# Kernel optimization log

Hardware: AMD Instinct MI355X
Metric: run time of the kernel (lower is better)

The kernel has to match this reference:

```python
import jax, jax.numpy as jnp
import numpy as np

V, E, H, D = 32000, 512, 512, 3          # vocab, embed_dim, hidden_dim, max_depth
PD = max(H // 4, 16)                      # policy depth-embed dim = 128
DEPTH_EMBED_SCALE = 0.01
SIB_SCALE = 1.0 / np.sqrt(H)              # sibling_scale default 1/sqrt(hidden_dim)
GREEDY_THRESHOLD = 0.5
PROB_MIN, PROB_MAX = 1e-7, 1.0 - 1e-7


def _ln(x, g, b, eps=1e-5):
    m = x.mean(-1, keepdims=True)
    v = jnp.var(x, axis=-1, keepdims=True)
    return (x - m) * jax.lax.rsqrt(v + eps) * g + b


def setup_inputs() -> dict:
    key = jax.random.key(0)
    ks = jax.random.split(key, 12)
    def n(k, shape, s=0.02):
        return jax.random.normal(k, shape, jnp.float32) * s
    return {
        "token_ids": jax.random.randint(ks[0], (4096,), 0, V),
        "emb": n(ks[1], (V, E)),                      # embedding table
        "proj_w": n(ks[2], (H, E), 0.04), "proj_b": jnp.zeros(H, jnp.float32),
        "cf_w": n(ks[3], (2 * H, H), 0.04), "cf_b": jnp.zeros(2 * H, jnp.float32),
        "in_g": jnp.ones(H, jnp.float32), "in_b": jnp.zeros(H, jnp.float32),   # policy input LayerNorm
        "pde": n(ks[4], (D + 1, PD), 0.01),           # policy depth embedding
        "f1w": n(ks[5], (H // 2, H + PD), 0.04), "f1b": jnp.zeros(H // 2, jnp.float32),
        "n1g": jnp.ones(H // 2, jnp.float32), "n1b": jnp.zeros(H // 2, jnp.float32),
        "f2w": n(ks[6], (H // 4, H // 2), 0.06), "f2b": jnp.zeros(H // 4, jnp.float32),
        "n2g": jnp.ones(H // 4, jnp.float32), "n2b": jnp.zeros(H // 4, jnp.float32),
        "pow_w": n(ks[7], (1, H // 4), 0.01), "pow_b": jnp.zeros(1, jnp.float32),
        "sib": n(ks[8], (2, H)),                      # sibling embeddings (left/right)
        "dep": n(ks[9], (D + 1, H), 0.01),            # tree depth embeddings
        "out_w": n(ks[10], (V, H), 0.04), "out_b": jnp.zeros(V, jnp.float32),
    }


def _forward(token_ids, emb, proj_w, proj_b, cf_w, cf_b, in_g, in_b, pde,
             f1w, f1b, n1g, n1b, f2w, f2b, n2g, n2b, pow_w, pow_b,
             sib, dep, out_w, out_b):
    # h0: project token embeddings to hidden space. [N, H]
    h0 = emb[token_ids] @ proj_w.T + proj_b
    nodes = h0[None]                      # level-0 nodes: [1, N, H]
    agg_sum = h0                          # running sum over all tree nodes
    agg_cnt = jnp.float32(1.0)
    alive = jnp.float32(1.0)              # cumulative greedy-expand mask
    for level in range(D):
        # growth policy on the level-mean hidden (+ scaled depth embedding)
        lh = nodes.mean(0) + DEPTH_EMBED_SCALE * dep[level]          # [N, H]
        hn = _ln(lh, in_g, in_b)
        de = jnp.broadcast_to(pde[min(level, D)], (hn.shape[0], PD))
        x = jnp.concatenate([hn, de], axis=-1)
        x = jax.nn.relu(_ln(x @ f1w.T + f1b, n1g, n1b))
        x = jax.nn.relu(_ln(x @ f2w.T + f2b, n2g, n2b))
        p = jax.nn.sigmoid((x @ pow_w.T + pow_b)[..., 0])             # [N]
        p_mean = jnp.clip(p, PROB_MIN, PROB_MAX).mean()
        alive = alive * (p_mean >= GREEDY_THRESHOLD).astype(jnp.float32)
        # binary child expansion: child_fc then chunk into left/right + sibling embeds
        cf = jnp.einsum('mnh,kh->mnk', nodes, cf_w) + cf_b            # [M, N, 2H]
        left = cf[..., :H] + SIB_SCALE * sib[0]
        right = cf[..., H:] + SIB_SCALE * sib[1]
        nodes = jnp.concatenate([left, right], axis=0)                # [2M, N, H]
        agg_sum = agg_sum + alive * nodes.sum(0)
        agg_cnt = agg_cnt + alive * jnp.float32(nodes.shape[0])
    pooled = agg_sum / jnp.maximum(agg_cnt, 1e-8)                     # mean pooling
    return pooled @ out_w.T + out_b                                   # [N, V]


def reference(token_ids, emb, proj_w, proj_b, cf_w, cf_b, in_g, in_b, pde,
              f1w, f1b, n1g, n1b, f2w, f2b, n2g, n2b, pow_w, pow_b,
              sib, dep, out_w, out_b):
    return _forward(token_ids, emb, proj_w, proj_b, cf_w, cf_b, in_g, in_b, pde,
                    f1w, f1b, n1g, n1b, f2w, f2b, n2g, n2b, pow_w, pow_b,
                    sib, dep, out_w, out_b)
```

## Files before the change

kernel.cpp:

```cpp
#include <hip/hip_runtime.h>

typedef unsigned short u16;
using bf16x8 = __attribute__((ext_vector_type(8))) short;
using f32x4  = __attribute__((ext_vector_type(4))) float;

#define SIB_SCALE_F 0.04419417382415922f

__device__ __forceinline__ u16 f2b(float f) {
  unsigned u = __builtin_bit_cast(unsigned, f);
  return (u16)((u + 0x7FFFu + ((u >> 16) & 1u)) >> 16);
}

__device__ __forceinline__ float wred(float v) {
  #pragma unroll
  for (int m = 1; m < 64; m <<= 1) v += __shfl_xor(v, m);
  return v;
}

__device__ __forceinline__ void gload16(const void* g, void* l) {
  __builtin_amdgcn_global_load_lds(
      (const __attribute__((address_space(1))) unsigned int*)g,
      (__attribute__((address_space(3))) unsigned int*)l, 16, 0, 0);
}

__global__ __launch_bounds__(512, 2) void gemm256_bt(
    const u16* __restrict__ A, const u16* __restrict__ B,
    const float* __restrict__ bias,
    float* __restrict__ C, int M, int N, int K)
{
  __shared__ u16 lds[65536];
  const int t = threadIdx.x, w = t >> 6, lane = t & 63;
  const int wm = w >> 2, wn = w & 3;
  const int r16 = lane & 15, ks = lane >> 4;

  const int nb = gridDim.x * gridDim.y;
  const int lid = blockIdx.y * gridDim.x + blockIdx.x;
  const int chunk = nb >> 3;
  const int nlid = (lid & 7) * chunk + (lid >> 3);
  const int bm = (nlid % gridDim.x) * 256;
  const int bn = (nlid / gridDim.x) * 256;

  const int NT = K >> 6;

  auto stageH = [&](const u16* __restrict__ G, int grow0, int kt, int half, int opBase) {
    const int k0 = kt << 6;
    u16* dst = lds + opBase + ((kt & 1) << 14) + (half << 13);
    #pragma unroll
    for (int j = 0; j < 2; ++j) {
      const int r = half * 128 + j * 64 + w * 8 + (lane >> 3);
      const int s = (lane & 7) ^ (r & 7);
      gload16(G + (size_t)(grow0 + r) * K + k0 + s * 8,
              dst + j * 4096 + w * 512);
    }
  };

  f32x4 acc[8][4];
  #pragma unroll
  for (int m = 0; m < 8; ++m)
    #pragma unroll
    for (int n = 0; n < 4; ++n) {
      f32x4 z = {0.f, 0.f, 0.f, 0.f};
      acc[m][n] = z;
    }

  stageH(A, bm, 0, 0, 0);
  stageH(A, bm, 0, 1, 0);
  stageH(B, bn, 0, 0, 32768);
  stageH(B, bn, 0, 1, 32768);
  if (NT > 1) {
    stageH(B, bn, 1, 0, 32768);
    stageH(B, bn, 1, 1, 32768);
    asm volatile("s_waitcnt vmcnt(4)" ::: "memory");
  } else {
    asm volatile("s_waitcnt vmcnt(0)" ::: "memory");
  }
  __builtin_amdgcn_sched_barrier(0);
  __builtin_amdgcn_s_barrier();

  for (int kt = 0; kt < NT; ++kt) {
    const u16* Ab = lds + ((kt & 1) << 14);
    const u16* Bb = lds + 32768 + ((kt & 1) << 14);
    bf16x8 bfr[4][2];

    #pragma unroll
    for (int p = 0; p < 4; ++p) {
      bf16x8 af2[2][2];
      #pragma unroll
      for (int i = 0; i < 2; ++i) {
        const int row = wm * 128 + (2 * p + i) * 16 + r16;
        af2[i][0] = *(const bf16x8*)(Ab + row * 64 + ((ks ^ (row & 7)) << 3));
        af2[i][1] = *(const bf16x8*)(Ab + row * 64 + (((4 + ks) ^ (row & 7)) << 3));
      }
      if (p == 0) {
        #pragma unroll
        for (int n = 0; n < 4; ++n) {
          const int row = wn * 64 + n * 16 + r16;
          bfr[n][0] = *(const bf16x8*)(Bb + row * 64 + ((ks ^ (row & 7)) << 3));
          bfr[n][1] = *(const bf16x8*)(Bb + row * 64 + (((4 + ks) ^ (row & 7)) << 3));
        }
      }
      if (p == 0 && kt + 1 < NT) stageH(A, bm, kt + 1, 0, 0);
      if (p == 1 && kt + 1 < NT) stageH(A, bm, kt + 1, 1, 0);
      if (p == 2 && kt + 2 < NT) stageH(B, bn, kt + 2, 0, 32768);
      if (p == 3) {
        if (kt + 2 < NT) {
          stageH(B, bn, kt + 2, 1, 32768);
          asm volatile("s_waitcnt vmcnt(4)" ::: "memory");
        } else {
          asm volatile("s_waitcnt vmcnt(0)" ::: "memory");
        }
        __builtin_amdgcn_sched_barrier(0);
      }
      __builtin_amdgcn_s_barrier();
      asm volatile("s_waitcnt lgkmcnt(0)" ::: "memory");
      __builtin_amdgcn_sched_barrier(0);
      __builtin_amdgcn_s_setprio(1);
      #pragma unroll
      for (int i = 0; i < 2; ++i)
        #pragma unroll
        for (int n = 0; n < 4; ++n) {
          acc[2 * p + i][n] = __builtin_amdgcn_mfma_f32_16x16x32_bf16(
              af2[i][0], bfr[n][0], acc[2 * p + i][n], 0, 0, 0);
          acc[2 * p + i][n] = __builtin_amdgcn_mfma_f32_16x16x32_bf16(
              af2[i][1], bfr[n][1], acc[2 * p + i][n], 0, 0, 0);
        }
      __builtin_amdgcn_s_setprio(0);
      __builtin_amdgcn_s_barrier();
    }
  }

  #pragma unroll
  for (int n = 0; n < 4; ++n) {
    const int gcol = bn + wn * 64 + n * 16 + r16;
    const float bv = bias[gcol];
    #pragma unroll
    for (int m = 0; m < 8; ++m) {
      const int grow0 = bm + wm * 128 + m * 16 + ks * 4;
      #pragma unroll
      for (int r = 0; r < 4; ++r)
        C[(size_t)(grow0 + r) * N + gcol] = acc[m][n][r] + bv;
    }
  }
}

template <bool GATHER>
__global__ __launch_bounds__(256) void gemm_bf16_bt(
    const float* __restrict__ Afp, const int* __restrict__ tok,
    const u16* __restrict__ A, const u16* __restrict__ B,
    const float* __restrict__ bias, int blvl, float bscale,
    float* __restrict__ C, u16* __restrict__ Cb,
    int M, int N, int K)
{
  __shared__ u16 ldsA[128 * 32];
  __shared__ u16 ldsB[128 * 32];
  const int t = threadIdx.x;
  const int w = t >> 6;
  const int lane = t & 63;
  const int wr = w >> 1, wc = w & 1;

  const int nb = gridDim.x * gridDim.y;
  const int lid = blockIdx.y * gridDim.x + blockIdx.x;
  const int chunk = nb >> 3;
  const int nlid = (lid & 7) * chunk + (lid >> 3);
  const int bx = nlid % gridDim.x, by = nlid / gridDim.x;

  const int bm = bx * 128, bn = by * 128;
  const int r16 = lane & 15, ks = lane >> 4;
  const int srow = t >> 2, sslot = t & 3;

  f32x4 acc[4][4];
  #pragma unroll
  for (int m = 0; m < 4; ++m)
    #pragma unroll
    for (int n = 0; n < 4; ++n) {
      f32x4 z = {0.f, 0.f, 0.f, 0.f};
      acc[m][n] = z;
    }

  for (int k0 = 0; k0 < K; k0 += 32) {
    if (k0) __syncthreads();
    #pragma unroll
    for (int i = 0; i < 2; ++i) {
      const int row = srow + i * 64;
      const int sl = sslot ^ ((row >> 1) & 3);
      if constexpr (GATHER) {
        const float* src = Afp + (size_t)tok[bm + row] * 512 + k0 + sl * 8;
        const float4 a0 = *(const float4*)src;
        const float4 a1 = *(const float4*)(src + 4);
        bf16x8 v;
        v[0] = (short)f2b(a0.x); v[1] = (short)f2b(a0.y);
        v[2] = (short)f2b(a0.z); v[3] = (short)f2b(a0.w);
        v[4] = (short)f2b(a1.x); v[5] = (short)f2b(a1.y);
        v[6] = (short)f2b(a1.z); v[7] = (short)f2b(a1.w);
        *(bf16x8*)(ldsA + i * 2048 + w * 512 + lane * 8) = v;
      } else {
        gload16(A + (size_t)(bm + row) * K + k0 + sl * 8,
                ldsA + (i * 2048 + w * 512));
      }
      gload16(B + (size_t)(bn + row) * K + k0 + sl * 8,
              ldsB + (i * 2048 + w * 512));
    }
    __syncthreads();

    bf16x8 af[4], bfr[4];
    #pragma unroll
    for (int m = 0; m < 4; ++m) {
      const int row = wr * 64 + m * 16 + r16;
      af[m] = *(const bf16x8*)(ldsA + row * 32 + ((ks ^ ((row >> 1) & 3)) << 3));
    }
    #pragma unroll
    for (int n = 0; n < 4; ++n) {
      const int row = wc * 64 + n * 16 + r16;
      bfr[n] = *(const bf16x8*)(ldsB + row * 32 + ((ks ^ ((row >> 1) & 3)) << 3));
    }
    #pragma unroll
    for (int m = 0; m < 4; ++m)
      #pragma unroll
      for (int n = 0; n < 4; ++n)
        acc[m][n] = __builtin_amdgcn_mfma_f32_16x16x32_bf16(af[m], bfr[n], acc[m][n], 0, 0, 0);
  }

  const float* be = bias + (size_t)(bm >> 12) * blvl;
  #pragma unroll
  for (int m = 0; m < 4; ++m) {
    const int grow0 = bm + wr * 64 + m * 16 + ks * 4;
    #pragma unroll
    for (int n = 0; n < 4; ++n) {
      const int gcol = bn + wc * 64 + n * 16 + r16;
      const float bv = be[gcol] * bscale;
      #pragma unroll
      for (int r = 0; r < 4; ++r) {
        const float v = acc[m][n][r] + bv;
        const size_t idx = (size_t)(grow0 + r) * N + gcol;
        C[idx] = v;
        if (Cb) Cb[idx] = f2b(v);
      }
    }
  }
}

__global__ __launch_bounds__(256) void prep_misc(
    const float* __restrict__ cf_w, const float* __restrict__ cf_b,
    const float* __restrict__ sib, const float* __restrict__ proj_w,
    const float* __restrict__ f1w, const float* __restrict__ f1b,
    const float* __restrict__ f2w, const float* __restrict__ pde,
    u16* __restrict__ wsum_b, u16* __restrict__ projw_b,
    u16* __restrict__ f1w512b, u16* __restrict__ f2wb,
    float* __restrict__ cvec, float* __restrict__ psum,
    float* __restrict__ y1bias)
{
  const int b = blockIdx.x, t = threadIdx.x;
  if (b < 256) {
    const int idx = b * 256 + t;
    const float4 a = ((const float4*)cf_w)[idx];
    const float4 c = ((const float4*)(cf_w + 262144))[idx];
    ushort4 o = { f2b(a.x + c.x), f2b(a.y + c.y), f2b(a.z + c.z), f2b(a.w + c.w) };
    ((ushort4*)wsum_b)[idx] = o;
  } else if (b < 512) {
    const int idx = (b - 256) * 256 + t;
    const float4 v = ((const float4*)proj_w)[idx];
    ushort4 o = { f2b(v.x), f2b(v.y), f2b(v.z), f2b(v.w) };
    ((ushort4*)projw_b)[idx] = o;
  } else if (b < 640) {
    const int fi = (b - 512) * 256 + t;
    const int row = fi >> 7, c4 = fi & 127;
    const float4 v = *(const float4*)(f1w + (size_t)row * 640 + c4 * 4);
    ushort4 o = { f2b(v.x), f2b(v.y), f2b(v.z), f2b(v.w) };
    ((ushort4*)f1w512b)[row * 128 + c4] = o;
  } else if (b < 672) {
    const int idx = (b - 640) * 256 + t;
    const float4 v = ((const float4*)f2w)[idx];
    ushort4 o = { f2b(v.x), f2b(v.y), f2b(v.z), f2b(v.w) };
    ((ushort4*)f2wb)[idx] = o;
  } else if (b < 675) {
    const int l = b - 672, j = t;
    const float* wrow = f1w + (size_t)j * 640 + 512;
    const float* p = pde + l * 128;
    float s = f1b[j];
    #pragma unroll 4
    for (int k = 0; k < 128; ++k) s += wrow[k] * p[k];
    y1bias[l * 256 + j] = s;
  } else {
    cvec[t]       = cf_b[t]       + cf_b[512 + t]       + SIB_SCALE_F * (sib[t]       + sib[512 + t]);
    cvec[256 + t] = cf_b[256 + t] + cf_b[768 + t] + SIB_SCALE_F * (sib[256 + t] + sib[768 + t]);
    if (t < 3) psum[t] = 0.f;
  }
}

__global__ __launch_bounds__(256) void mean_ln_concat_b(
    const float* __restrict__ S0, const float* __restrict__ S1,
    const float* __restrict__ S2,
    const float* __restrict__ dep,
    const float* __restrict__ g, const float* __restrict__ b,
    u16* __restrict__ X)
{
  const int wid = threadIdx.x >> 6, lane = threadIdx.x & 63;
  const int gr = blockIdx.x * 4 + wid;
  const int l = gr >> 12, n = gr & 4095;
  const float* Sr = (l == 0 ? S0 : l == 1 ? S1 : S2) + (size_t)n * 512;
  const float invM = (l == 0 ? 1.f : l == 1 ? 0.5f : 0.25f);
  const float* depl = dep + 512 * l;
  const int c0 = lane * 8;
  float x[8];
  float s = 0.f, sq = 0.f;
  #pragma unroll
  for (int i = 0; i < 8; ++i) {
    const float v = Sr[c0 + i] * invM + 0.01f * depl[c0 + i];
    x[i] = v; s += v; sq += v * v;
  }
  s = wred(s); sq = wred(sq);
  const float mean = s * (1.f / 512.f);
  const float var = sq * (1.f / 512.f) - mean * mean;
  const float rs = rsqrtf(var + 1e-5f);
  ushort4 o0, o1;
  o0.x = f2b((x[0] - mean) * rs * g[c0 + 0] + b[c0 + 0]);
  o0.y = f2b((x[1] - mean) * rs * g[c0 + 1] + b[c0 + 1]);
  o0.z = f2b((x[2] - mean) * rs * g[c0 + 2] + b[c0 + 2]);
  o0.w = f2b((x[3] - mean) * rs * g[c0 + 3] + b[c0 + 3]);
  o1.x = f2b((x[4] - mean) * rs * g[c0 + 4] + b[c0 + 4]);
  o1.y = f2b((x[5] - mean) * rs * g[c0 + 5] + b[c0 + 5]);
  o1.z = f2b((x[6] - mean) * rs * g[c0 + 6] + b[c0 + 6]);
  o1.w = f2b((x[7] - mean) * rs * g[c0 + 7] + b[c0 + 7]);
  ushort4* Xr = (ushort4*)(X + (size_t)gr * 512);
  Xr[lane * 2]     = o0;
  Xr[lane * 2 + 1] = o1;
}

__global__ __launch_bounds__(256) void ln_relu_b256(
    const float* __restrict__ X, const float* __restrict__ g,
    const float* __restrict__ b, u16* __restrict__ O)
{
  const int wid = threadIdx.x >> 6, lane = threadIdx.x & 63;
  const int n = blockIdx.x * 4 + wid;
  const float* Xr = X + (size_t)n * 256;
  float x[4];
  float s = 0.f, sq = 0.f;
  #pragma unroll
  for (int i = 0; i < 4; ++i) {
    x[i] = Xr[lane * 4 + i]; s += x[i]; sq += x[i] * x[i];
  }
  s = wred(s); sq = wred(sq);
  const float mean = s * (1.f / 256.f);
  const float var = sq * (1.f / 256.f) - mean * mean;
  const float rs = rsqrtf(var + 1e-5f);
  ushort4 o;
  o.x = f2b(fmaxf((x[0] - mean) * rs * g[lane * 4 + 0] + b[lane * 4 + 0], 0.f));
  o.y = f2b(fmaxf((x[1] - mean) * rs * g[lane * 4 + 1] + b[lane * 4 + 1], 0.f));
  o.z = f2b(fmaxf((x[2] - mean) * rs * g[lane * 4 + 2] + b[lane * 4 + 2], 0.f));
  o.w = f2b(fmaxf((x[3] - mean) * rs * g[lane * 4 + 3] + b[lane * 4 + 3], 0.f));
  ((ushort4*)(O + (size_t)n * 256))[lane] = o;
}

__global__ __launch_bounds__(256) void ln_relu128(
    float* __restrict__ X, const float* __restrict__ g, const float* __restrict__ b)
{
  const int wid = threadIdx.x >> 6, lane = threadIdx.x & 63;
  const int n = blockIdx.x * 4 + wid;
  float* Xr = X + (size_t)n * 128;
  float x[2];
  float s = 0.f, sq = 0.f;
  #pragma unroll
  for (int i = 0; i < 2; ++i) {
    x[i] = Xr[lane * 2 + i]; s += x[i]; sq += x[i] * x[i];
  }
  s = wred(s); sq = wred(sq);
  const float mean = s * (1.f / 128.f);
  const float var = sq * (1.f / 128.f) - mean * mean;
  const float rs = rsqrtf(var + 1e-5f);
  #pragma unroll
  for (int i = 0; i < 2; ++i) {
    const int c = lane * 2 + i;
    Xr[c] = fmaxf((x[i] - mean) * rs * g[c] + b[c], 0.f);
  }
}

__global__ __launch_bounds__(256) void policy_reduce_b(
    const float* __restrict__ Y2, const float* __restrict__ pw,
    const float* __restrict__ pb, float* __restrict__ psum)
{
  __shared__ float part[4];
  const int wid = threadIdx.x >> 6, lane = threadIdx.x & 63;
  const int gr = blockIdx.x * 4 + wid;
  const float* r = Y2 + (size_t)gr * 128;
  float z = r[lane * 2] * pw[lane * 2] + r[lane * 2 + 1] * pw[lane * 2 + 1];
  z = wred(z);
  if (lane == 0) {
    const float p = 1.f / (1.f + expf(-(z + pb[0])));
    part[wid] = fminf(fmaxf(p, 1e-7f), 1.f - 1e-7f);
  }
  __syncthreads();
  if (threadIdx.x == 0)
    atomicAdd(psum + (gr >> 12), part[0] + part[1] + part[2] + part[3]);
}

__global__ void finalize_coef(const float* __restrict__ psum, float* __restrict__ coef)
{
  float alive = 1.f, cnt = 1.f;
  #pragma unroll
  for (int l = 0; l < 3; ++l) {
    const float pm = psum[l] * (1.f / 4096.f);
    if (!(pm >= 0.5f)) alive = 0.f;
    coef[l] = alive;
    cnt += alive * (float)(2 << l);
  }
  coef[3] = 1.f / fmaxf(cnt, 1e-8f);
}

__global__ __launch_bounds__(256) void pool_to_bf16(
    const float* __restrict__ h0, const float* __restrict__ S1,
    const float* __restrict__ S2, const float* __restrict__ S3,
    const float* __restrict__ coef, u16* __restrict__ P)
{
  const int idx = blockIdx.x * 256 + threadIdx.x;
  const float c0 = coef[0], c1 = coef[1], c2 = coef[2], inv = coef[3];
  const float4 a  = ((const float4*)h0)[idx];
  const float4 s1 = ((const float4*)S1)[idx];
  const float4 s2 = ((const float4*)S2)[idx];
  const float4 s3 = ((const float4*)S3)[idx];
  ushort4 o;
  o.x = f2b((a.x + c0 * s1.x + c1 * s2.x + c2 * s3.x) * inv);
  o.y = f2b((a.y + c0 * s1.y + c1 * s2.y + c2 * s3.y) * inv);
  o.z = f2b((a.z + c0 * s1.z + c1 * s2.z + c2 * s3.z) * inv);
  o.w = f2b((a.w + c0 * s1.w + c1 * s2.w + c2 * s3.w) * inv);
  ((ushort4*)P)[idx] = o;
}

__global__ __launch_bounds__(256) void f32_to_bf16_vec(
    const float* __restrict__ src, u16* __restrict__ dst, int n4)
{
  const int idx = blockIdx.x * 256 + threadIdx.x;
  if (idx >= n4) return;
  const float4 v = ((const float4*)src)[idx];
  ushort4 o = { f2b(v.x), f2b(v.y), f2b(v.z), f2b(v.w) };
  ((ushort4*)dst)[idx] = o;
}

extern "C" void kernel_launch(void* const* d_in, const int* in_sizes, int n_in,
                              void* d_out, int out_size, void* d_ws, size_t ws_size,
                              hipStream_t stream) {
  const int*   tok    = (const int*)  d_in[0];
  const float* emb    = (const float*)d_in[1];
  const float* proj_w = (const float*)d_in[2];
  const float* proj_b = (const float*)d_in[3];
  const float* cf_w   = (const float*)d_in[4];
  const float* cf_b   = (const float*)d_in[5];
  const float* in_g   = (const float*)d_in[6];
  const float* in_b   = (const float*)d_in[7];
  const float* pde    = (const float*)d_in[8];
  const float* f1w    = (const float*)d_in[9];
  const float* f1b    = (const float*)d_in[10];
  const float* n1g    = (const float*)d_in[11];
  const float* n1b    = (const float*)d_in[12];
  const float* f2w    = (const float*)d_in[13];
  const float* f2bias = (const float*)d_in[14];
  const float* n2g    = (const float*)d_in[15];
  const float* n2b    = (const float*)d_in[16];
  const float* pow_w  = (const float*)d_in[17];
  const float* pow_b  = (const float*)d_in[18];
  const float* sib    = (const float*)d_in[19];
  const float* dep    = (const float*)d_in[20];
  const float* out_w  = (const float*)d_in[21];
  const float* out_b  = (const float*)d_in[22];
  float* out = (float*)d_out;

  char* ws = (char*)d_ws;
  size_t off = 0;
  auto alloc = [&](size_t bytes) -> void* {
    void* p = ws + off;
    off += (bytes + 255) & ~(size_t)255;
    return p;
  };
  u16*   outw_b  = (u16*)  alloc((size_t)32000 * 512 * 2);
  u16*   projw_b = (u16*)  alloc((size_t)512 * 512 * 2);
  u16*   wsum_b  = (u16*)  alloc((size_t)512 * 512 * 2);
  u16*   f1w512b = (u16*)  alloc((size_t)256 * 512 * 2);
  u16*   f2wb    = (u16*)  alloc((size_t)128 * 256 * 2);
  float* h0f     = (float*)alloc((size_t)4096 * 512 * 4);
  u16*   h0b     = (u16*)  alloc((size_t)4096 * 512 * 2);
  float* S1f     = (float*)alloc((size_t)4096 * 512 * 4);
  u16*   S1b     = (u16*)  alloc((size_t)4096 * 512 * 2);
  float* S2f     = (float*)alloc((size_t)4096 * 512 * 4);
  u16*   S2b     = (u16*)  alloc((size_t)4096 * 512 * 2);
  float* S3f     = (float*)alloc((size_t)4096 * 512 * 4);
  u16*   S3b     = (u16*)  alloc((size_t)4096 * 512 * 2);
  u16*   X       = (u16*)  alloc((size_t)12288 * 512 * 2);
  float* Y1      = (float*)alloc((size_t)12288 * 256 * 4);
  u16*   Y1b     = (u16*)  alloc((size_t)12288 * 256 * 2);
  float* Y2      = (float*)alloc((size_t)12288 * 128 * 4);
  float* y1bias  = (float*)alloc(3 * 256 * 4);
  float* cvec    = (float*)alloc(512 * 4);
  float* psum    = (float*)alloc(256);
  float* coef    = (float*)alloc(256);
  u16*   poolb   = (u16*)  alloc((size_t)4096 * 512 * 2);

  prep_misc<<<676, 256, 0, stream>>>(cf_w, cf_b, sib, proj_w, f1w, f1b, f2w, pde,
                                     wsum_b, projw_b, f1w512b, f2wb,
                                     cvec, psum, y1bias);
  f32_to_bf16_vec<<<16000, 256, 0, stream>>>(out_w, outw_b, 4096000);

  gemm_bf16_bt<true><<<dim3(32, 4), 256, 0, stream>>>(
      emb, tok, nullptr, projw_b, proj_b, 0, 1.f, h0f, h0b, 4096, 512, 512);
  gemm_bf16_bt<false><<<dim3(32, 4), 256, 0, stream>>>(
      nullptr, nullptr, h0b, wsum_b, cvec, 0, 1.f, S1f, S1b, 4096, 512, 512);
  gemm_bf16_bt<false><<<dim3(32, 4), 256, 0, stream>>>(
      nullptr, nullptr, S1b, wsum_b, cvec, 0, 2.f, S2f, S2b, 4096, 512, 512);
  gemm_bf16_bt<false><<<dim3(32, 4), 256, 0, stream>>>(
      nullptr, nullptr, S2b, wsum_b, cvec, 0, 4.f, S3f, S3b, 4096, 512, 512);

  mean_ln_concat_b<<<3072, 256, 0, stream>>>(h0f, S1f, S2f, dep, in_g, in_b, X);
  gemm_bf16_bt<false><<<dim3(96, 2), 256, 0, stream>>>(
      nullptr, nullptr, X, f1w512b, y1bias, 256, 1.f, Y1, nullptr, 12288, 256, 512);
  ln_relu_b256<<<3072, 256, 0, stream>>>(Y1, n1g, n1b, Y1b);
  gemm_bf16_bt<false><<<dim3(96, 1), 256, 0, stream>>>(
      nullptr, nullptr, Y1b, f2wb, f2bias, 0, 1.f, Y2, nullptr, 12288, 128, 256);
  ln_relu128<<<3072, 256, 0, stream>>>(Y2, n2g, n2b);
  policy_reduce_b<<<3072, 256, 0, stream>>>(Y2, pow_w, pow_b, psum);
  finalize_coef<<<1, 1, 0, stream>>>(psum, coef);

  pool_to_bf16<<<2048, 256, 0, stream>>>(h0f, S1f, S2f, S3f, coef, poolb);

  gemm256_bt<<<dim3(16, 125), 512, 0, stream>>>(poolb, outw_b, out_b,
                                                out, 4096, 32000, 512);
}
```

Before: 448.5 us.

## Shrink GEMM tiles to raise occupancy and block count across all GEMMs

```diff
diff --git a/kernel.cpp b/kernel.cpp
--- a/kernel.cpp
+++ b/kernel.cpp
@@ -23,12 +23,12 @@
       (__attribute__((address_space(3))) unsigned int*)l, 16, 0, 0);
 }
 
-__global__ __launch_bounds__(512, 2) void gemm256_bt(
+__global__ __launch_bounds__(512, 4) void gemmF(
     const u16* __restrict__ A, const u16* __restrict__ B,
     const float* __restrict__ bias,
     float* __restrict__ C, int M, int N, int K)
 {
-  __shared__ u16 lds[65536];
+  __shared__ u16 lds[28672];
   const int t = threadIdx.x, w = t >> 6, lane = t & 63;
   const int wm = w >> 2, wn = w & 3;
   const int r16 = lane & 15, ks = lane >> 4;
@@ -37,96 +37,93 @@
   const int lid = blockIdx.y * gridDim.x + blockIdx.x;
   const int chunk = nb >> 3;
   const int nlid = (lid & 7) * chunk + (lid >> 3);
-  const int bm = (nlid % gridDim.x) * 256;
+  const int bm = (nlid % gridDim.x) * 128;
   const int bn = (nlid / gridDim.x) * 256;
 
-  const int NT = K >> 6;
-
-  auto stageH = [&](const u16* __restrict__ G, int grow0, int kt, int half, int opBase) {
-    const int k0 = kt << 6;
-    u16* dst = lds + opBase + ((kt & 1) << 14) + (half << 13);
+  const int NT = K >> 5;
+  const int srow = lane >> 2, sslot = lane & 3;
+
+  auto stageA = [&](int kt) {
+    const int row = w * 16 + srow;
+    const int s = sslot ^ ((row >> 1) & 3);
+    gload16(A + (size_t)(bm + row) * K + (kt << 5) + s * 8,
+            lds + (kt % 3) * 4096 + w * 512);
+  };
+  auto stageB = [&](int kt) {
     #pragma unroll
     for (int j = 0; j < 2; ++j) {
-      const int r = half * 128 + j * 64 + w * 8 + (lane >> 3);
-      const int s = (lane & 7) ^ (r & 7);
-      gload16(G + (size_t)(grow0 + r) * K + k0 + s * 8,
-              dst + j * 4096 + w * 512);
+      const int row = j * 128 + w * 16 + srow;
+      const int s = sslot ^ ((row >> 1) & 3);
+      gload16(B + (size_t)(bn + row) * K + (kt << 5) + s * 8,
+              lds + 12288 + (kt & 1) * 8192 + j * 4096 + w * 512);
     }
   };
 
-  f32x4 acc[8][4];
-  #pragma unroll
-  for (int m = 0; m < 8; ++m)
+  f32x4 acc[4][4];
+  #pragma unroll
+  for (int m = 0; m < 4; ++m)
     #pragma unroll
     for (int n = 0; n < 4; ++n) {
       f32x4 z = {0.f, 0.f, 0.f, 0.f};
       acc[m][n] = z;
     }
 
-  stageH(A, bm, 0, 0, 0);
-  stageH(A, bm, 0, 1, 0);
-  stageH(B, bn, 0, 0, 32768);
-  stageH(B, bn, 0, 1, 32768);
-  if (NT > 1) {
-    stageH(B, bn, 1, 0, 32768);
-    stageH(B, bn, 1, 1, 32768);
-    asm volatile("s_waitcnt vmcnt(4)" ::: "memory");
-  } else {
-    asm volatile("s_waitcnt vmcnt(0)" ::: "memory");
-  }
+  stageA(0); stageB(0); stageA(1); stageB(1);
+  asm volatile("s_waitcnt vmcnt(3)" ::: "memory");
   __builtin_amdgcn_sched_barrier(0);
   __builtin_amdgcn_s_barrier();
 
   for (int kt = 0; kt < NT; ++kt) {
-    const u16* Ab = lds + ((kt & 1) << 14);
-    const u16* Bb = lds + 32768 + ((kt & 1) << 14);
-    bf16x8 bfr[4][2];
-
-    #pragma unroll
-    for (int p = 0; p < 4; ++p) {
-      bf16x8 af2[2][2];
+    const u16* Ab = lds + (kt % 3) * 4096;
+    const u16* Bb = lds + 12288 + (kt & 1) * 8192;
+    bf16x8 bfr[4], af[2];
+
+    #pragma unroll
+    for (int i = 0; i < 2; ++i) {
+      const int row = wm * 64 + i * 16 + r16;
+      af[i] = *(const bf16x8*)(Ab + row * 32 + ((ks ^ ((row >> 1) & 3)) << 3));
+    }
+    #pragma unroll
+    for (int n = 0; n < 4; ++n) {
+      const int row = wn * 64 + n * 16 + r16;
+      bfr[n] = *(const bf16x8*)(Bb + row * 32 + ((ks ^ ((row >> 1) & 3)) << 3));
+    }
+    if (kt + 2 < NT) stageA(kt + 2);
+    __builtin_amdgcn_s_barrier();
+    asm volatile("s_waitcnt lgkmcnt(0)" ::: "memory");
+    __builtin_amdgcn_sched_barrier(0);
+    __builtin_amdgcn_s_setprio(1);
+    #pragma unroll
+    for (int i = 0; i < 2; ++i)
       #pragma unroll
-      for (int i = 0; i < 2; ++i) {
-        const int row = wm * 128 + (2 * p + i) * 16 + r16;
-        af2[i][0] = *(const bf16x8*)(Ab + row * 64 + ((ks ^ (row & 7)) << 3));
-        af2[i][1] = *(const bf16x8*)(Ab + row * 64 + (((4 + ks) ^ (row & 7)) << 3));
-      }
-      if (p == 0) {
-        #pragma unroll
-        for (int n = 0; n < 4; ++n) {
-          const int row = wn * 64 + n * 16 + r16;
-          bfr[n][0] = *(const bf16x8*)(Bb + row * 64 + ((ks ^ (row & 7)) << 3));
-          bfr[n][1] = *(const bf16x8*)(Bb + row * 64 + (((4 + ks) ^ (row & 7)) << 3));
-        }
-      }
-      if (p == 0 && kt + 1 < NT) stageH(A, bm, kt + 1, 0, 0);
-      if (p == 1 && kt + 1 < NT) stageH(A, bm, kt + 1, 1, 0);
-      if (p == 2 && kt + 2 < NT) stageH(B, bn, kt + 2, 0, 32768);
-      if (p == 3) {
-        if (kt + 2 < NT) {
-          stageH(B, bn, kt + 2, 1, 32768);
-          asm volatile("s_waitcnt vmcnt(4)" ::: "memory");
-        } else {
-          asm volatile("s_waitcnt vmcnt(0)" ::: "memory");
-        }
-        __builtin_amdgcn_sched_barrier(0);
-      }
-      __builtin_amdgcn_s_barrier();
-      asm volatile("s_waitcnt lgkmcnt(0)" ::: "memory");
-      __builtin_amdgcn_sched_barrier(0);
-      __builtin_amdgcn_s_setprio(1);
+      for (int n = 0; n < 4; ++n)
+        acc[i][n] = __builtin_amdgcn_mfma_f32_16x16x32_bf16(af[i], bfr[n], acc[i][n], 0, 0, 0);
+    __builtin_amdgcn_s_setprio(0);
+    __builtin_amdgcn_s_barrier();
+
+    #pragma unroll
+    for (int i = 0; i < 2; ++i) {
+      const int row = wm * 64 + (2 + i) * 16 + r16;
+      af[i] = *(const bf16x8*)(Ab + row * 32 + ((ks ^ ((row >> 1) & 3)) << 3));
+    }
+    if (kt + 2 < NT) {
+      stageB(kt + 2);
+      asm volatile("s_waitcnt vmcnt(3)" ::: "memory");
+    } else {
+      asm volatile("s_waitcnt vmcnt(0)" ::: "memory");
+    }
+    __builtin_amdgcn_sched_barrier(0);
+    __builtin_amdgcn_s_barrier();
+    asm volatile("s_waitcnt lgkmcnt(0)" ::: "memory");
+    __builtin_amdgcn_sched_barrier(0);
+    __builtin_amdgcn_s_setprio(1);
+    #pragma unroll
+    for (int i = 0; i < 2; ++i)
       #pragma unroll
-      for (int i = 0; i < 2; ++i)
-        #pragma unroll
-        for (int n = 0; n < 4; ++n) {
-          acc[2 * p + i][n] = __builtin_amdgcn_mfma_f32_16x16x32_bf16(
-              af2[i][0], bfr[n][0], acc[2 * p + i][n], 0, 0, 0);
-          acc[2 * p + i][n] = __builtin_amdgcn_mfma_f32_16x16x32_bf16(
-              af2[i][1], bfr[n][1], acc[2 * p + i][n], 0, 0, 0);
-        }
-      __builtin_amdgcn_s_setprio(0);
-      __builtin_amdgcn_s_barrier();
-    }
+      for (int n = 0; n < 4; ++n)
+        acc[2 + i][n] = __builtin_amdgcn_mfma_f32_16x16x32_bf16(af[i], bfr[n], acc[2 + i][n], 0, 0, 0);
+    __builtin_amdgcn_s_setprio(0);
+    __builtin_amdgcn_s_barrier();
   }
 
   #pragma unroll
@@ -134,8 +131,8 @@
     const int gcol = bn + wn * 64 + n * 16 + r16;
     const float bv = bias[gcol];
     #pragma unroll
-    for (int m = 0; m < 8; ++m) {
-      const int grow0 = bm + wm * 128 + m * 16 + ks * 4;
+    for (int m = 0; m < 4; ++m) {
+      const int grow0 = bm + wm * 64 + m * 16 + ks * 4;
       #pragma unroll
       for (int r = 0; r < 4; ++r)
         C[(size_t)(grow0 + r) * N + gcol] = acc[m][n][r] + bv;
@@ -144,44 +141,40 @@
 }
 
 template <bool GATHER>
-__global__ __launch_bounds__(256) void gemm_bf16_bt(
+__global__ __launch_bounds__(256) void gemm64(
     const float* __restrict__ Afp, const int* __restrict__ tok,
     const u16* __restrict__ A, const u16* __restrict__ B,
     const float* __restrict__ bias, int blvl, float bscale,
     float* __restrict__ C, u16* __restrict__ Cb,
     int M, int N, int K)
 {
-  __shared__ u16 ldsA[128 * 32];
+  __shared__ u16 ldsA[64 * 32];
   __shared__ u16 ldsB[128 * 32];
-  const int t = threadIdx.x;
-  const int w = t >> 6;
-  const int lane = t & 63;
-  const int wr = w >> 1, wc = w & 1;
+  const int t = threadIdx.x, w = t >> 6, lane = t & 63;
+  const int r16 = lane & 15, ks = lane >> 4;
 
   const int nb = gridDim.x * gridDim.y;
   const int lid = blockIdx.y * gridDim.x + blockIdx.x;
   const int chunk = nb >> 3;
   const int nlid = (lid & 7) * chunk + (lid >> 3);
-  const int bx = nlid % gridDim.x, by = nlid / gridDim.x;
-
-  const int bm = bx * 128, bn = by * 128;
-  const int r16 = lane & 15, ks = lane >> 4;
+  const int bm = (nlid % gridDim.x) * 64;
+  const int bn = (nlid / gridDim.x) * 128;
+
   const int srow = t >> 2, sslot = t & 3;
 
-  f32x4 acc[4][4];
+  f32x4 acc[4][2];
   #pragma unroll
   for (int m = 0; m < 4; ++m)
     #pragma unroll
-    for (int n = 0; n < 4; ++n) {
+    for (int n = 0; n < 2; ++n) {
       f32x4 z = {0.f, 0.f, 0.f, 0.f};
       acc[m][n] = z;
     }
 
   for (int k0 = 0; k0 < K; k0 += 32) {
     if (k0) __syncthreads();
-    #pragma unroll
-    for (int i = 0; i < 2; ++i) {
-      const int row = srow + i * 64;
+    {
+      const int row = srow;
       const int sl = sslot ^ ((row >> 1) & 3);
       if constexpr (GATHER) {
         const float* src = Afp + (size_t)tok[bm + row] * 512 + k0 + sl * 8;
@@ -192,41 +185,45 @@
         v[2] = (short)f2b(a0.z); v[3] = (short)f2b(a0.w);
         v[4] = (short)f2b(a1.x); v[5] = (short)f2b(a1.y);
         v[6] = (short)f2b(a1.z); v[7] = (short)f2b(a1.w);
-        *(bf16x8*)(ldsA + i * 2048 + w * 512 + lane * 8) = v;
+        *(bf16x8*)(ldsA + t * 8) = v;
       } else {
-        gload16(A + (size_t)(bm + row) * K + k0 + sl * 8,
-                ldsA + (i * 2048 + w * 512));
+        gload16(A + (size_t)(bm + row) * K + k0 + sl * 8, ldsA + w * 512);
       }
+    }
+    #pragma unroll
+    for (int i = 0; i < 2; ++i) {
+      const int row = i * 64 + srow;
+      const int sl = sslot ^ ((row >> 1) & 3);
       gload16(B + (size_t)(bn + row) * K + k0 + sl * 8,
-              ldsB + (i * 2048 + w * 512));
+              ldsB + i * 2048 + w * 512);
     }
     __syncthreads();
 
-    bf16x8 af[4], bfr[4];
+    bf16x8 af[4], bfr[2];
     #pragma unroll
     for (int m = 0; m < 4; ++m) {
-      const int row = wr * 64 + m * 16 + r16;
+      const int row = m * 16 + r16;
       af[m] = *(const bf16x8*)(ldsA + row * 32 + ((ks ^ ((row >> 1) & 3)) << 3));
     }
     #pragma unroll
-    for (int n = 0; n < 4; ++n) {
-      const int row = wc * 64 + n * 16 + r16;
+    for (int n = 0; n < 2; ++n) {
+      const int row = w * 32 + n * 16 + r16;
       bfr[n] = *(const bf16x8*)(ldsB + row * 32 + ((ks ^ ((row >> 1) & 3)) << 3));
     }
     #pragma unroll
     for (int m = 0; m < 4; ++m)
       #pragma unroll
-      for (int n = 0; n < 4; ++n)
+      for (int n = 0; n < 2; ++n)
         acc[m][n] = __builtin_amdgcn_mfma_f32_16x16x32_bf16(af[m], bfr[n], acc[m][n], 0, 0, 0);
   }
 
   const float* be = bias + (size_t)(bm >> 12) * blvl;
   #pragma unroll
   for (int m = 0; m < 4; ++m) {
-    const int grow0 = bm + wr * 64 + m * 16 + ks * 4;
-    #pragma unroll
-    for (int n = 0; n < 4; ++n) {
-      const int gcol = bn + wc * 64 + n * 16 + r16;
+    const int grow0 = bm + m * 16 + ks * 4;
+    #pragma unroll
+    for (int n = 0; n < 2; ++n) {
+      const int gcol = bn + w * 32 + n * 16 + r16;
       const float bv = be[gcol] * bscale;
       #pragma unroll
       for (int r = 0; r < 4; ++r) {
@@ -281,7 +278,7 @@
     for (int k = 0; k < 128; ++k) s += wrow[k] * p[k];
     y1bias[l * 256 + j] = s;
   } else {
-    cvec[t]       = cf_b[t]       + cf_b[512 + t]       + SIB_SCALE_F * (sib[t]       + sib[512 + t]);
+    cvec[t]       = cf_b[t]       + cf_b[512 + t] + SIB_SCALE_F * (sib[t]       + sib[512 + t]);
     cvec[256 + t] = cf_b[256 + t] + cf_b[768 + t] + SIB_SCALE_F * (sib[256 + t] + sib[768 + t]);
     if (t < 3) psum[t] = 0.f;
   }
@@ -498,20 +495,20 @@
                                      cvec, psum, y1bias);
   f32_to_bf16_vec<<<16000, 256, 0, stream>>>(out_w, outw_b, 4096000);
 
-  gemm_bf16_bt<true><<<dim3(32, 4), 256, 0, stream>>>(
+  gemm64<true><<<dim3(64, 4), 256, 0, stream>>>(
       emb, tok, nullptr, projw_b, proj_b, 0, 1.f, h0f, h0b, 4096, 512, 512);
-  gemm_bf16_bt<false><<<dim3(32, 4), 256, 0, stream>>>(
+  gemm64<false><<<dim3(64, 4), 256, 0, stream>>>(
       nullptr, nullptr, h0b, wsum_b, cvec, 0, 1.f, S1f, S1b, 4096, 512, 512);
-  gemm_bf16_bt<false><<<dim3(32, 4), 256, 0, stream>>>(
+  gemm64<false><<<dim3(64, 4), 256, 0, stream>>>(
       nullptr, nullptr, S1b, wsum_b, cvec, 0, 2.f, S2f, S2b, 4096, 512, 512);
-  gemm_bf16_bt<false><<<dim3(32, 4), 256, 0, stream>>>(
+  gemm64<false><<<dim3(64, 4), 256, 0, stream>>>(
       nullptr, nullptr, S2b, wsum_b, cvec, 0, 4.f, S3f, S3b, 4096, 512, 512);
 
   mean_ln_concat_b<<<3072, 256, 0, stream>>>(h0f, S1f, S2f, dep, in_g, in_b, X);
-  gemm_bf16_bt<false><<<dim3(96, 2), 256, 0, stream>>>(
+  gemm64<false><<<dim3(192, 2), 256, 0, stream>>>(
       nullptr, nullptr, X, f1w512b, y1bias, 256, 1.f, Y1, nullptr, 12288, 256, 512);
   ln_relu_b256<<<3072, 256, 0, stream>>>(Y1, n1g, n1b, Y1b);
-  gemm_bf16_bt<false><<<dim3(96, 1), 256, 0, stream>>>(
+  gemm64<false><<<dim3(192, 1), 256, 0, stream>>>(
       nullptr, nullptr, Y1b, f2wb, f2bias, 0, 1.f, Y2, nullptr, 12288, 128, 256);
   ln_relu128<<<3072, 256, 0, stream>>>(Y2, n2g, n2b);
   policy_reduce_b<<<3072, 256, 0, stream>>>(Y2, pow_w, pow_b, psum);
@@ -519,6 +516,6 @@
 
   pool_to_bf16<<<2048, 256, 0, stream>>>(h0f, S1f, S2f, S3f, coef, poolb);
 
-  gemm256_bt<<<dim3(16, 125), 512, 0, stream>>>(poolb, outw_b, out_b,
-                                                out, 4096, 32000, 512);
-}
+  gemmF<<<dim3(32, 125), 512, 0, stream>>>(poolb, outw_b, out_b,
+                                           out, 4096, 32000, 512);
+}
```

Result: slower. 463.2 us (+3.3%).
